# Optimization experiments

Hardware: AMD Instinct MI355X
Metric: run time of the kernel (lower is better)

## Reference

```python
import jax, jax.numpy as jnp
import numpy as np

HQ, HKV, HD = 16, 4, 64  # q heads, kv heads, head dim
ROPE_BASE = 10000.0


def _rope_tables(n, dim):
    inv_freq = 1.0 / (ROPE_BASE ** (jnp.arange(0, dim, 2, dtype=jnp.float32) / dim))
    t = jnp.arange(n, dtype=jnp.float32)
    freqs = jnp.outer(t, inv_freq)           # [N, dim/2]
    emb = jnp.concatenate([freqs, freqs], -1)  # [N, dim]
    return jnp.cos(emb), jnp.sin(emb)


def _rotate_half(x):
    h = x.shape[-1] // 2
    return jnp.concatenate([-x[..., h:], x[..., :h]], axis=-1)


def _apply_rope(x, cos, sin):
    # x: [B, N, H, D]; cos/sin: [N, D]
    c = cos[None, :, None, :]
    s = sin[None, :, None, :]
    return x * c + _rotate_half(x) * s


def setup_inputs() -> dict:
    key = jax.random.key(0)
    ks = jax.random.split(key, 5)
    B, N, D = 2, 4096, 1024
    kvD = HKV * HD
    sc = 0.02
    return {
        "x": jax.random.normal(ks[0], (B, N, D), jnp.float32),
        "Wq": jax.random.normal(ks[1], (D, D), jnp.float32) * sc,
        "Wk": jax.random.normal(ks[2], (D, kvD), jnp.float32) * sc,
        "Wv": jax.random.normal(ks[3], (D, kvD), jnp.float32) * sc,
        "Wo": jax.random.normal(ks[4], (D, D), jnp.float32) * sc,
    }


def reference(x, Wq, Wk, Wv, Wo):
    B, N, D = x.shape
    G = HQ // HKV
    Q = (x @ Wq).reshape(B, N, HQ, HD)
    K = (x @ Wk).reshape(B, N, HKV, HD)
    V = (x @ Wv).reshape(B, N, HKV, HD)

    cos, sin = _rope_tables(N, HD)
    Q = _apply_rope(Q, cos, sin)
    K = _apply_rope(K, cos, sin)

    # GQA: expand KV heads to match Q heads (repeat_interleave over head dim)
    K = jnp.repeat(K, G, axis=2)  # [B, N, HQ, HD]
    V = jnp.repeat(V, G, axis=2)

    Q = Q.transpose(0, 2, 1, 3)  # [B, HQ, N, HD]
    K = K.transpose(0, 2, 1, 3)
    V = V.transpose(0, 2, 1, 3)

    scores = jnp.einsum('bhqd,bhkd->bhqk', Q, K) / jnp.sqrt(jnp.float32(HD))
    attn = jax.nn.softmax(scores, axis=-1)
    out = jnp.einsum('bhqk,bhkd->bhqd', attn, V)  # [B, HQ, N, HD]
    out = out.transpose(0, 2, 1, 3).reshape(B, N, D)
    return out @ Wo
```

## Files before the change

kernel.cpp:

```cpp
#include <hip/hip_runtime.h>

#define HQn   16
#define HKVn  4
#define HDn   64
#define SEQN  4096
#define NB    2
#define DM    1024
#define KVD   256
#define NPACK 1536

#define QSCALE 0.18033688011112042f

typedef __attribute__((ext_vector_type(8))) short short8;
typedef __attribute__((ext_vector_type(4))) float f32x4;

#define MFMA16 __builtin_amdgcn_mfma_f32_16x16x32_bf16
#define EXP2F(x) __builtin_amdgcn_exp2f(x)

static __device__ __forceinline__ unsigned short f2bf(float f){
  union { float f; unsigned int u; } c; c.f = f;
  unsigned int r = c.u + 0x7fffu + ((c.u >> 16) & 1u);
  return (unsigned short)(r >> 16);
}

#if __has_builtin(__builtin_amdgcn_cvt_pk_bf16_f32)
typedef __attribute__((ext_vector_type(2))) __bf16 bf16x2v;
static __device__ __forceinline__ unsigned int pk_bf2(float a, float b){
  union { bf16x2v v; unsigned int u; } c;
  c.v = __builtin_amdgcn_cvt_pk_bf16_f32(a, b);
  return c.u;
}
#else
static __device__ __forceinline__ unsigned int pk_bf2(float a, float b){
  union { float f; unsigned int u; } ca, cb; ca.f = a; cb.f = b;
  return ((ca.u + 0x8000u) >> 16) | ((cb.u + 0x8000u) & 0xFFFF0000u);
}
#endif

static __device__ __forceinline__ void swap32pair(unsigned a, unsigned b, int lane,
                                                  unsigned &o0, unsigned &o1){
#if __has_builtin(__builtin_amdgcn_permlane32_swap)
  auto r = __builtin_amdgcn_permlane32_swap(a, b, false, false);
  o0 = r[0]; o1 = r[1];
#else
  int ax = ((lane ^ 32) & 63) * 4;
  unsigned as = __builtin_amdgcn_ds_bpermute(ax, a);
  unsigned bs = __builtin_amdgcn_ds_bpermute(ax, b);
  o0 = (lane < 32) ? a  : bs;
  o1 = (lane < 32) ? as : b;
#endif
}
static __device__ __forceinline__ void swap16pair(unsigned x, unsigned y, int lane,
                                                  unsigned &o0, unsigned &o1){
#if __has_builtin(__builtin_amdgcn_permlane16_swap)
  auto r = __builtin_amdgcn_permlane16_swap(x, y, false, false);
  o0 = r[0]; o1 = r[1];
#else
  int ax = ((lane ^ 16) & 63) * 4;
  unsigned xs = __builtin_amdgcn_ds_bpermute(ax, x);
  unsigned ys = __builtin_amdgcn_ds_bpermute(ax, y);
  bool odd = (lane >> 4) & 1;
  o0 = odd ? ys : x;
  o1 = odd ? y  : xs;
#endif
}

static __device__ __forceinline__ void gl2lds16(const void* g, void* l){
  __builtin_amdgcn_global_load_lds(
      (const __attribute__((address_space(1))) void*)g,
      (__attribute__((address_space(3))) void*)l, 16, 0, 0);
}

__global__ void rope_tables_k(float* __restrict__ ct, float* __restrict__ st){
  int t = blockIdx.x, d = threadIdx.x;
  int i = d & 31;
  float inv = 1.0f / powf(10000.0f, (float)i * (1.0f/32.0f));
  float ang = (float)t * inv;
  ct[t*HDn + d] = cosf(ang);
  st[t*HDn + d] = sinf(ang);
}

__global__ __launch_bounds__(256) void castx_k(const float* __restrict__ x,
                                               unsigned short* __restrict__ xb){
  size_t i = ((size_t)blockIdx.x * 256 + threadIdx.x) * 8;
  float4 a = *(const float4*)(x + i);
  float4 b = *(const float4*)(x + i + 4);
  short8 o;
  o[0]=f2bf(a.x); o[1]=f2bf(a.y); o[2]=f2bf(a.z); o[3]=f2bf(a.w);
  o[4]=f2bf(b.x); o[5]=f2bf(b.y); o[6]=f2bf(b.z); o[7]=f2bf(b.w);
  *(short8*)(xb + i) = o;
}

__global__ __launch_bounds__(256) void castw_k(
    const float* __restrict__ Wq, const float* __restrict__ Wk,
    const float* __restrict__ Wv, const float* __restrict__ Wo,
    unsigned short* __restrict__ Wqkv_t, unsigned short* __restrict__ Wot)
{
  const int z = blockIdx.z;
  const float* W; unsigned short* D; int srcN, nOff;
  if      (z == 0) { W = Wq; D = Wqkv_t; srcN = DM;  nOff = 0;    }
  else if (z == 1) { W = Wo; D = Wot;    srcN = DM;  nOff = 0;    }
  else if (z == 2) { W = Wk; D = Wqkv_t; srcN = KVD; nOff = 1024; }
  else             { W = Wv; D = Wqkv_t; srcN = KVD; nOff = 1280; }
  const int n0 = blockIdx.y * 64;
  if (n0 >= srcN) return;
  const int k0 = blockIdx.x * 64;
  const int tid = threadIdx.x;

  __shared__ float tile[64][65];
  const int lr = tid >> 4, lc = (tid & 15) * 4;
  #pragma unroll
  for (int p = 0; p < 4; p++) {
    float4 v = *(const float4*)&W[(size_t)(k0 + lr + p*16) * srcN + n0 + lc];
    tile[lr + p*16][lc+0] = v.x; tile[lr + p*16][lc+1] = v.y;
    tile[lr + p*16][lc+2] = v.z; tile[lr + p*16][lc+3] = v.w;
  }
  __syncthreads();

  const int nn = tid >> 2, kc = (tid & 3) * 16;
  unsigned short* dp = D + (size_t)(nOff + n0 + nn) * DM + k0 + kc;
  #pragma unroll
  for (int q = 0; q < 4; q++) {
    ushort4 o;
    o.x = f2bf(tile[kc + q*4 + 0][nn]);
    o.y = f2bf(tile[kc + q*4 + 1][nn]);
    o.z = f2bf(tile[kc + q*4 + 2][nn]);
    o.w = f2bf(tile[kc + q*4 + 3][nn]);
    *(ushort4*)(dp + q*4) = o;
  }
}

__global__ __launch_bounds__(256) void qkv2_k(
    const unsigned short* __restrict__ A, const unsigned short* __restrict__ Bt,
    const float* __restrict__ ct, const float* __restrict__ st,
    unsigned short* __restrict__ Qo, unsigned short* __restrict__ Ko,
    unsigned short* __restrict__ Vo)
{
  __shared__ __align__(16) short As[128][32];
  __shared__ __align__(16) short Bs[128][32];

  const int m0 = blockIdx.x * 128, n0 = blockIdx.y * 128;
  const int tid = threadIdx.x, lane = tid & 63, w = tid >> 6;
  const int wm = w >> 1, wn = w & 1;
  const int ln = lane & 15, quad = lane >> 4;

  f32x4 acc[4][4];
  #pragma unroll
  for (int i = 0; i < 4; i++)
    #pragma unroll
    for (int j = 0; j < 4; j++) acc[i][j] = (f32x4){0.f,0.f,0.f,0.f};

  const int r0 = tid >> 2, c8 = (tid & 3) * 8;
  const int r1 = r0 + 64;

  for (int k0 = 0; k0 < DM; k0 += 32) {
    gl2lds16(A  + (size_t)(m0 + r0)*DM + k0 + c8, &As[r0][c8]);
    gl2lds16(A  + (size_t)(m0 + r1)*DM + k0 + c8, &As[r1][c8]);
    gl2lds16(Bt + (size_t)(n0 + r0)*DM + k0 + c8, &Bs[r0][c8]);
    gl2lds16(Bt + (size_t)(n0 + r1)*DM + k0 + c8, &Bs[r1][c8]);
    __syncthreads();

    short8 af[4], bf[4];
    #pragma unroll
    for (int mb = 0; mb < 4; mb++) af[mb] = *(const short8*)&As[wm*64 + mb*16 + ln][quad*8];
    #pragma unroll
    for (int nb = 0; nb < 4; nb++) bf[nb] = *(const short8*)&Bs[wn*64 + nb*16 + ln][quad*8];
    #pragma unroll
    for (int mb = 0; mb < 4; mb++)
      #pragma unroll
      for (int nb = 0; nb < 4; nb++)
        acc[mb][nb] = MFMA16(af[mb], bf[nb], acc[mb][nb], 0, 0, 0);
    __syncthreads();
  }

  const int nc = n0 + wn*64;
  int kind, head;
  if (nc < 1024)      { kind = 0; head = nc >> 6;          }
  else if (nc < 1280) { kind = 1; head = (nc - 1024) >> 6; }
  else                { kind = 2; head = (nc - 1280) >> 6; }

  if (kind == 2) {
    #pragma unroll
    for (int mb = 0; mb < 4; mb++) {
      const int m = m0 + wm*64 + mb*16 + quad*4;
      const int t = m & (SEQN-1), b = m >> 12;
      #pragma unroll
      for (int nb = 0; nb < 4; nb++) {
        int d = nb*16 + ln;
        ushort4 pk;
        pk.x = f2bf(acc[mb][nb][0]); pk.y = f2bf(acc[mb][nb][1]);
        pk.z = f2bf(acc[mb][nb][2]); pk.w = f2bf(acc[mb][nb][3]);
        *(ushort4*)&Vo[(((size_t)(b*HKVn + head))*HDn + d)*SEQN + t] = pk;
      }
    }
  } else {
    #pragma unroll
    for (int mb = 0; mb < 4; mb++) {
      #pragma unroll
      for (int nb = 0; nb < 4; nb++) {
        #pragma unroll
        for (int r = 0; r < 4; r++) {
          int m = m0 + wm*64 + mb*16 + quad*4 + r;
          int t = m & (SEQN-1), b = m >> 12;
          int d = nb*16 + ln;
          float v = acc[mb][nb][r];
          float partner = (nb < 2) ? -acc[mb][nb+2][r] : acc[mb][nb-2][r];
          float cv = ct[t*HDn + d], sv = st[t*HDn + d];
          float o = v*cv + partner*sv;
          if (kind == 0) Qo[(((size_t)(b*HQn  + head))*SEQN + t)*HDn + d] = f2bf(o * QSCALE);
          else           Ko[(((size_t)(b*HKVn + head))*SEQN + t)*HDn + d] = f2bf(o);
        }
      }
    }
  }
}

__global__ __launch_bounds__(256, 4) void attn_k(
    const unsigned short* __restrict__ Q, const unsigned short* __restrict__ K,
    const unsigned short* __restrict__ Vt, unsigned short* __restrict__ AO)
{
  __shared__ short kls[4][16][72];
  __shared__ short vts[64][72];

  const int id  = blockIdx.x;
  const int bhv = id & 7;
  const int b   = bhv >> 2, hv = bhv & 3;
  const int rem = id >> 3;
  const int qt  = rem & 31;
  const int h   = hv*4 + (rem >> 5);
  const int q0  = qt * 128;

  const int tid = threadIdx.x, lane = tid & 63, w = tid >> 6;
  const int ln = lane & 15, quad = lane >> 4;

  const unsigned short* Qp = Q + (((size_t)(b*HQn + h))*SEQN + q0 + w*32) * HDn;
  const unsigned short* Kp = K + ((size_t)(b*HKVn + hv))*SEQN * HDn;
  const unsigned short* Vp = Vt + ((size_t)(b*HKVn + hv))*HDn * SEQN;

  short8 qf[2][2];
  qf[0][0] = *(const short8*)(Qp + ln*HDn + quad*8);
  qf[0][1] = *(const short8*)(Qp + ln*HDn + 32 + quad*8);
  qf[1][0] = *(const short8*)(Qp + (16+ln)*HDn + quad*8);
  qf[1][1] = *(const short8*)(Qp + (16+ln)*HDn + 32 + quad*8);

  short8 ones;
  #pragma unroll
  for (int j = 0; j < 8; j++) ones[j] = (short)0x3F80;

  f32x4 o[2][4], lacc[2];
  #pragma unroll
  for (int g = 0; g < 2; g++) {
    #pragma unroll
    for (int i = 0; i < 4; i++) o[g][i] = (f32x4){0.f,0.f,0.f,0.f};
    lacc[g] = (f32x4){0.f,0.f,0.f,0.f};
  }

  const int j0 = tid >> 3, sc0 = (tid & 7) * 8;
  const int j1 = j0 + 32;

  for (int kt = 0; kt < SEQN; kt += 64) {
    *(short8*)&kls[j0 & 3][j0 >> 2][sc0] = *(const short8*)(Kp + (size_t)(kt + j0)*HDn + sc0);
    *(short8*)&kls[j1 & 3][j1 >> 2][sc0] = *(const short8*)(Kp + (size_t)(kt + j1)*HDn + sc0);
    *(short8*)&vts[j0][sc0] = *(const short8*)(Vp + (size_t)j0*SEQN + kt + sc0);
    *(short8*)&vts[j1][sc0] = *(const short8*)(Vp + (size_t)j1*SEQN + kt + sc0);
    __syncthreads();

    f32x4 s[2][4];
    #pragma unroll
    for (int nb = 0; nb < 4; nb++) {
      short8 k0 = *(const short8*)&kls[nb][ln][     quad*8];
      short8 k1 = *(const short8*)&kls[nb][ln][32 + quad*8];
      f32x4 t0 = (f32x4){0.f,0.f,0.f,0.f};
      t0 = MFMA16(k0, qf[0][0], t0, 0, 0, 0);
      t0 = MFMA16(k1, qf[0][1], t0, 0, 0, 0);
      s[0][nb] = t0;
      f32x4 t1 = (f32x4){0.f,0.f,0.f,0.f};
      t1 = MFMA16(k0, qf[1][0], t1, 0, 0, 0);
      t1 = MFMA16(k1, qf[1][1], t1, 0, 0, 0);
      s[1][nb] = t1;
    }

    short8 pf[2][2];
    #pragma unroll
    for (int g = 0; g < 2; g++) {
      unsigned u0[4], u1[4];
      #pragma unroll
      for (int r = 0; r < 4; r++) {
        u0[r] = pk_bf2(EXP2F(s[g][0][r]), EXP2F(s[g][1][r]));
        u1[r] = pk_bf2(EXP2F(s[g][2][r]), EXP2F(s[g][3][r]));
      }
      union { short8 s8; unsigned u[4]; } f0, f1;
      #pragma unroll
      for (int rho = 0; rho < 2; rho++) {
        unsigned a0, a1, t0, t1;
        swap16pair(u0[rho], u0[rho+2], lane, a0, a1);
        swap32pair(a0, a1, lane, t0, t1);
        f0.u[2*rho+0] = t0; f1.u[2*rho+0] = t1;
        swap16pair(u1[rho], u1[rho+2], lane, a0, a1);
        swap32pair(a0, a1, lane, t0, t1);
        f0.u[2*rho+1] = t0; f1.u[2*rho+1] = t1;
      }
      pf[g][0] = f0.s8; pf[g][1] = f1.s8;
    }

    #pragma unroll
    for (int db = 0; db < 4; db++) {
      short8 v0 = *(const short8*)&vts[db*16 + ln][     quad*8];
      short8 v1 = *(const short8*)&vts[db*16 + ln][32 + quad*8];
      o[0][db] = MFMA16(pf[0][0], v0, o[0][db], 0, 0, 0);
      o[0][db] = MFMA16(pf[0][1], v1, o[0][db], 0, 0, 0);
      o[1][db] = MFMA16(pf[1][0], v0, o[1][db], 0, 0, 0);
      o[1][db] = MFMA16(pf[1][1], v1, o[1][db], 0, 0, 0);
    }
    lacc[0] = MFMA16(pf[0][0], ones, lacc[0], 0, 0, 0);
    lacc[0] = MFMA16(pf[0][1], ones, lacc[0], 0, 0, 0);
    lacc[1] = MFMA16(pf[1][0], ones, lacc[1], 0, 0, 0);
    lacc[1] = MFMA16(pf[1][1], ones, lacc[1], 0, 0, 0);
    __syncthreads();
  }

  #pragma unroll
  for (int g = 0; g < 2; g++) {
    float inv[4];
    #pragma unroll
    for (int r = 0; r < 4; r++) inv[r] = 1.0f / lacc[g][r];
    #pragma unroll
    for (int db = 0; db < 4; db++) {
      #pragma unroll
      for (int r = 0; r < 4; r++) {
        int gq = q0 + w*32 + g*16 + quad*4 + r;
        int d  = db*16 + ln;
        AO[(((size_t)(b*SEQN + gq))*HQn + h)*HDn + d] = f2bf(o[g][db][r] * inv[r]);
      }
    }
  }
}

__global__ __launch_bounds__(256) void oproj2_k(
    const unsigned short* __restrict__ A, const unsigned short* __restrict__ Bt,
    float* __restrict__ out)
{
  __shared__ __align__(16) short As[128][32];
  __shared__ __align__(16) short Bs[128][32];

  const int m0 = blockIdx.x * 128, n0 = blockIdx.y * 128;
  const int tid = threadIdx.x, lane = tid & 63, w = tid >> 6;
  const int wm = w >> 1, wn = w & 1;
  const int ln = lane & 15, quad = lane >> 4;

  f32x4 acc[4][4];
  #pragma unroll
  for (int i = 0; i < 4; i++)
    #pragma unroll
    for (int j = 0; j < 4; j++) acc[i][j] = (f32x4){0.f,0.f,0.f,0.f};

  const int r0 = tid >> 2, c8 = (tid & 3) * 8;
  const int r1 = r0 + 64;

  for (int k0 = 0; k0 < DM; k0 += 32) {
    gl2lds16(A  + (size_t)(m0 + r0)*DM + k0 + c8, &As[r0][c8]);
    gl2lds16(A  + (size_t)(m0 + r1)*DM + k0 + c8, &As[r1][c8]);
    gl2lds16(Bt + (size_t)(n0 + r0)*DM + k0 + c8, &Bs[r0][c8]);
    gl2lds16(Bt + (size_t)(n0 + r1)*DM + k0 + c8, &Bs[r1][c8]);
    __syncthreads();

    short8 af[4], bf[4];
    #pragma unroll
    for (int mb = 0; mb < 4; mb++) af[mb] = *(const short8*)&As[wm*64 + mb*16 + ln][quad*8];
    #pragma unroll
    for (int nb = 0; nb < 4; nb++) bf[nb] = *(const short8*)&Bs[wn*64 + nb*16 + ln][quad*8];
    #pragma unroll
    for (int mb = 0; mb < 4; mb++)
      #pragma unroll
      for (int nb = 0; nb < 4; nb++)
        acc[mb][nb] = MFMA16(af[mb], bf[nb], acc[mb][nb], 0, 0, 0);
    __syncthreads();
  }

  #pragma unroll
  for (int mb = 0; mb < 4; mb++) {
    #pragma unroll
    for (int nb = 0; nb < 4; nb++) {
      #pragma unroll
      for (int r = 0; r < 4; r++) {
        int m = m0 + wm*64 + mb*16 + quad*4 + r;
        int c = n0 + wn*64 + nb*16 + ln;
        out[(size_t)m*DM + c] = acc[mb][nb][r];
      }
    }
  }
}

extern "C" void kernel_launch(void* const* d_in, const int* in_sizes, int n_in,
                              void* d_out, int out_size, void* d_ws, size_t ws_size,
                              hipStream_t stream) {
  const float* x  = (const float*)d_in[0];
  const float* Wq = (const float*)d_in[1];
  const float* Wk = (const float*)d_in[2];
  const float* Wv = (const float*)d_in[3];
  const float* Wo = (const float*)d_in[4];
  float* out = (float*)d_out;

  char* ws = (char*)d_ws;
  float* cos_t = (float*)ws;
  float* sin_t = cos_t + SEQN*HDn;
  unsigned short* xb     = (unsigned short*)(sin_t + SEQN*HDn);
  unsigned short* AO     = xb;
  unsigned short* Wqkv_t = xb + (size_t)NB*SEQN*DM;
  unsigned short* Wot    = Wqkv_t + (size_t)NPACK*DM;
  unsigned short* Qb     = Wot + (size_t)DM*DM;
  unsigned short* Kb     = Qb + (size_t)NB*HQn *SEQN*HDn;
  unsigned short* Vb     = Kb + (size_t)NB*HKVn*SEQN*HDn;

  hipLaunchKernelGGL(rope_tables_k, dim3(SEQN), dim3(HDn), 0, stream, cos_t, sin_t);
  hipLaunchKernelGGL(castx_k, dim3((NB*SEQN*DM)/(256*8)), dim3(256), 0, stream, x, xb);
  hipLaunchKernelGGL(castw_k, dim3(16, 16, 4), dim3(256), 0, stream,
                     Wq, Wk, Wv, Wo, Wqkv_t, Wot);
  hipLaunchKernelGGL(qkv2_k, dim3(64, 12), dim3(256), 0, stream,
                     xb, Wqkv_t, cos_t, sin_t, Qb, Kb, Vb);
  hipLaunchKernelGGL(attn_k, dim3(1024), dim3(256), 0, stream,
                     Qb, Kb, Vb, AO);
  hipLaunchKernelGGL(oproj2_k, dim3(64, 8), dim3(256), 0, stream,
                     AO, Wot, out);
}
```

Baseline: 321.6 us.

## Double-buffer K/V tiles in LDS with register prefetch in attention loop

The attention kernel now keeps two LDS buffers for K and V tiles. The next tile's global loads are issued into registers before the current tile's compute, and only one barrier per iteration remains instead of two. The intent is to hide global memory latency behind the MFMA work and cut synchronisation. In exchange it doubles the LDS footprint, which may reduce occupancy, and it adds live registers for the prefetch.

```diff
diff --git a/kernel.cpp b/kernel.cpp
--- a/kernel.cpp
+++ b/kernel.cpp
@@ -219,8 +219,8 @@
     const unsigned short* __restrict__ Q, const unsigned short* __restrict__ K,
     const unsigned short* __restrict__ Vt, unsigned short* __restrict__ AO)
 {
-  __shared__ short kls[4][16][72];
-  __shared__ short vts[64][72];
+  __shared__ short kls[2][4][16][72];
+  __shared__ short vts[2][64][72];
 
   const int id  = blockIdx.x;
   const int bhv = id & 7;
@@ -258,18 +258,34 @@
   const int j0 = tid >> 3, sc0 = (tid & 7) * 8;
   const int j1 = j0 + 32;
 
+  short8 rk0 = *(const short8*)(Kp + (size_t)j0*HDn + sc0);
+  short8 rk1 = *(const short8*)(Kp + (size_t)j1*HDn + sc0);
+  short8 rv0 = *(const short8*)(Vp + (size_t)j0*SEQN + sc0);
+  short8 rv1 = *(const short8*)(Vp + (size_t)j1*SEQN + sc0);
+
+  int c = 0;
   for (int kt = 0; kt < SEQN; kt += 64) {
-    *(short8*)&kls[j0 & 3][j0 >> 2][sc0] = *(const short8*)(Kp + (size_t)(kt + j0)*HDn + sc0);
-    *(short8*)&kls[j1 & 3][j1 >> 2][sc0] = *(const short8*)(Kp + (size_t)(kt + j1)*HDn + sc0);
-    *(short8*)&vts[j0][sc0] = *(const short8*)(Vp + (size_t)j0*SEQN + kt + sc0);
-    *(short8*)&vts[j1][sc0] = *(const short8*)(Vp + (size_t)j1*SEQN + kt + sc0);
-    __syncthreads();
+    *(short8*)&kls[c][j0 & 3][j0 >> 2][sc0] = rk0;
+    *(short8*)&kls[c][j1 & 3][j1 >> 2][sc0] = rk1;
+    *(short8*)&vts[c][j0][sc0] = rv0;
+    *(short8*)&vts[c][j1][sc0] = rv1;
+    asm volatile("s_waitcnt lgkmcnt(0)" ::: "memory");
+
+    {
+      const int ktn = (kt + 64) & (SEQN - 1);
+      rk0 = *(const short8*)(Kp + (size_t)(ktn + j0)*HDn + sc0);
+      rk1 = *(const short8*)(Kp + (size_t)(ktn + j1)*HDn + sc0);
+      rv0 = *(const short8*)(Vp + (size_t)j0*SEQN + ktn + sc0);
+      rv1 = *(const short8*)(Vp + (size_t)j1*SEQN + ktn + sc0);
+    }
+    __builtin_amdgcn_sched_barrier(0);
+    __builtin_amdgcn_s_barrier();
 
     f32x4 s[2][4];
     #pragma unroll
     for (int nb = 0; nb < 4; nb++) {
-      short8 k0 = *(const short8*)&kls[nb][ln][     quad*8];
-      short8 k1 = *(const short8*)&kls[nb][ln][32 + quad*8];
+      short8 k0 = *(const short8*)&kls[c][nb][ln][     quad*8];
+      short8 k1 = *(const short8*)&kls[c][nb][ln][32 + quad*8];
       f32x4 t0 = (f32x4){0.f,0.f,0.f,0.f};
       t0 = MFMA16(k0, qf[0][0], t0, 0, 0, 0);
       t0 = MFMA16(k1, qf[0][1], t0, 0, 0, 0);
@@ -305,8 +321,8 @@
 
     #pragma unroll
     for (int db = 0; db < 4; db++) {
-      short8 v0 = *(const short8*)&vts[db*16 + ln][     quad*8];
-      short8 v1 = *(const short8*)&vts[db*16 + ln][32 + quad*8];
+      short8 v0 = *(const short8*)&vts[c][db*16 + ln][     quad*8];
+      short8 v1 = *(const short8*)&vts[c][db*16 + ln][32 + quad*8];
       o[0][db] = MFMA16(pf[0][0], v0, o[0][db], 0, 0, 0);
       o[0][db] = MFMA16(pf[0][1], v1, o[0][db], 0, 0, 0);
       o[1][db] = MFMA16(pf[1][0], v0, o[1][db], 0, 0, 0);
@@ -316,7 +332,8 @@
     lacc[0] = MFMA16(pf[0][1], ones, lacc[0], 0, 0, 0);
     lacc[1] = MFMA16(pf[1][0], ones, lacc[1], 0, 0, 0);
     lacc[1] = MFMA16(pf[1][1], ones, lacc[1], 0, 0, 0);
-    __syncthreads();
+
+    c ^= 1;
   }
 
   #pragma unroll
```

After: 334.1 us. 3.9% more time.

## Double-buffer K/V tiles with direct global-to-LDS loads and XOR swizzle

Applied to the files above, without the earlier changes.

The attention kernel now stages K and V tiles straight from global memory into LDS through an async global-to-LDS helper. Two waves load K and two load V, each tile is double-buffered, and the next tile is prefetched while the current one is computed. The padded LDS layout is replaced by an XOR-swizzled 64x64 layout to avoid bank conflicts without padding. The aim is to hide global load latency behind the MFMA work and drop the register round-trip. The cost is twice the LDS footprint, which could limit occupancy.

```diff
diff --git a/kernel.cpp b/kernel.cpp
--- a/kernel.cpp
+++ b/kernel.cpp
@@ -219,8 +219,8 @@
     const unsigned short* __restrict__ Q, const unsigned short* __restrict__ K,
     const unsigned short* __restrict__ Vt, unsigned short* __restrict__ AO)
 {
-  __shared__ short kls[4][16][72];
-  __shared__ short vts[64][72];
+  __shared__ __align__(16) short kb[2][64][64];
+  __shared__ __align__(16) short vb[2][64][64];
 
   const int id  = blockIdx.x;
   const int bhv = id & 7;
@@ -255,21 +255,49 @@
     lacc[g] = (f32x4){0.f,0.f,0.f,0.f};
   }
 
-  const int j0 = tid >> 3, sc0 = (tid & 7) * 8;
-  const int j1 = j0 + 32;
-
+  const int w2   = w & 1;
+  const int lrow = lane >> 3;
+  const int slin = lane & 7;
+  const int sK   = slin ^ lrow;
+
+  int kkey[4]; size_t vrow[4];
+  #pragma unroll
+  for (int i = 0; i < 4; i++) {
+    const int row = w2*32 + i*8 + lrow;
+    kkey[i] = 4*(row & 15) + (row >> 4);
+    vrow[i] = (size_t)row * SEQN;
+  }
+
+  #define STAGE(cn, kts)                                                     \
+    do {                                                                     \
+      if (w < 2) {                                                           \
+        _Pragma("unroll")                                                    \
+        for (int i = 0; i < 4; i++)                                          \
+          gl2lds16(Kp + (size_t)((kts) + kkey[i])*HDn + sK*8,                \
+                   &kb[cn][w2*32 + i*8][0]);                                 \
+      } else {                                                               \
+        _Pragma("unroll")                                                    \
+        for (int i = 0; i < 4; i++)                                          \
+          gl2lds16(Vp + vrow[i] + (kts) + sK*8,                              \
+                   &vb[cn][w2*32 + i*8][0]);                                 \
+      }                                                                      \
+    } while (0)
+
+  const int swz0 = (( quad      ^ (ln & 7)) * 8);
+  const int swz1 = (((quad + 4) ^ (ln & 7)) * 8);
+
+  STAGE(0, 0);
+  __syncthreads();
+
+  int c = 0;
   for (int kt = 0; kt < SEQN; kt += 64) {
-    *(short8*)&kls[j0 & 3][j0 >> 2][sc0] = *(const short8*)(Kp + (size_t)(kt + j0)*HDn + sc0);
-    *(short8*)&kls[j1 & 3][j1 >> 2][sc0] = *(const short8*)(Kp + (size_t)(kt + j1)*HDn + sc0);
-    *(short8*)&vts[j0][sc0] = *(const short8*)(Vp + (size_t)j0*SEQN + kt + sc0);
-    *(short8*)&vts[j1][sc0] = *(const short8*)(Vp + (size_t)j1*SEQN + kt + sc0);
-    __syncthreads();
+    if (kt + 64 < SEQN) STAGE(c ^ 1, kt + 64);
 
     f32x4 s[2][4];
     #pragma unroll
     for (int nb = 0; nb < 4; nb++) {
-      short8 k0 = *(const short8*)&kls[nb][ln][     quad*8];
-      short8 k1 = *(const short8*)&kls[nb][ln][32 + quad*8];
+      short8 k0 = *(const short8*)&kb[c][nb*16 + ln][swz0];
+      short8 k1 = *(const short8*)&kb[c][nb*16 + ln][swz1];
       f32x4 t0 = (f32x4){0.f,0.f,0.f,0.f};
       t0 = MFMA16(k0, qf[0][0], t0, 0, 0, 0);
       t0 = MFMA16(k1, qf[0][1], t0, 0, 0, 0);
@@ -305,8 +333,8 @@
 
     #pragma unroll
     for (int db = 0; db < 4; db++) {
-      short8 v0 = *(const short8*)&vts[db*16 + ln][     quad*8];
-      short8 v1 = *(const short8*)&vts[db*16 + ln][32 + quad*8];
+      short8 v0 = *(const short8*)&vb[c][db*16 + ln][swz0];
+      short8 v1 = *(const short8*)&vb[c][db*16 + ln][swz1];
       o[0][db] = MFMA16(pf[0][0], v0, o[0][db], 0, 0, 0);
       o[0][db] = MFMA16(pf[0][1], v1, o[0][db], 0, 0, 0);
       o[1][db] = MFMA16(pf[1][0], v0, o[1][db], 0, 0, 0);
@@ -316,8 +344,11 @@
     lacc[0] = MFMA16(pf[0][1], ones, lacc[0], 0, 0, 0);
     lacc[1] = MFMA16(pf[1][0], ones, lacc[1], 0, 0, 0);
     lacc[1] = MFMA16(pf[1][1], ones, lacc[1], 0, 0, 0);
+
     __syncthreads();
-  }
+    c ^= 1;
+  }
+  #undef STAGE
 
   #pragma unroll
   for (int g = 0; g < 2; g++) {
```

Measured after the change: 324.5 us. About the same (+0.9%).
